# Performance work log

Measured on AMD Instinct MI355X. Metric: run time of the kernel, lower is better.

The kernel has to match this reference:

```python
import jax, jax.numpy as jnp
import numpy as np

N, E, F, H, HEADS, L, G = 16384, 262144, 16, 128, 4, 5, 128
DFF = 4 * H
EPS = 1e-5

def _bn(h, g, b):
    m = h.mean(axis=0)
    v = h.var(axis=0)
    return g * (h - m) / jnp.sqrt(v + EPS) + b

def setup_inputs():
    key = jax.random.key(0)
    ks = jax.random.split(key, 20)
    rn = lambda k, s, fan: jax.random.normal(k, s, jnp.float32) / np.float32(np.sqrt(fan))
    return {
        'x': jax.random.normal(ks[0], (N, F), jnp.float32),
        'edge_index': jax.random.randint(ks[1], (2, E), 0, N),
        'batch_index': jnp.sort(jax.random.randint(ks[2], (N,), 0, G)),
        'embW': rn(ks[3], (F, H), F), 'embb': jnp.zeros((H,), jnp.float32),
        'emb_g': jnp.ones((H,), jnp.float32), 'emb_be': jnp.zeros((H,), jnp.float32),
        'Wq': rn(ks[4], (L, H, HEADS * H), H), 'bq': jnp.zeros((L, HEADS * H), jnp.float32),
        'Wk': rn(ks[5], (L, H, HEADS * H), H), 'bk': jnp.zeros((L, HEADS * H), jnp.float32),
        'Wv': rn(ks[6], (L, H, HEADS * H), H), 'bv': jnp.zeros((L, HEADS * H), jnp.float32),
        'Wskip': rn(ks[7], (L, H, H), H), 'bskip': jnp.zeros((L, H), jnp.float32),
        'Wbeta': rn(ks[8], (L, 3 * H, 1), 3 * H),
        'W1': rn(ks[9], (L, H, DFF), H), 'b1': jnp.zeros((L, DFF), jnp.float32),
        'g1': jnp.ones((L, DFF), jnp.float32), 'be1': jnp.zeros((L, DFF), jnp.float32),
        'W2': rn(ks[10], (L, DFF, H), DFF), 'b2': jnp.zeros((L, H), jnp.float32),
        'predW': rn(ks[11], (H, 1), H), 'predb': jnp.zeros((1,), jnp.float32),
    }

def reference(x, edge_index, batch_index, embW, embb, emb_g, emb_be, Wq, bq, Wk, bk, Wv, bv, Wskip, bskip, Wbeta, W1, b1, g1, be1, W2, b2, predW, predb):
    src, dst = edge_index[0], edge_index[1]
    h = jax.nn.gelu(_bn(x @ embW + embb, emb_g, emb_be), approximate=False)
    scale = jnp.float32(1.0 / np.sqrt(H))  # sqrt(out_channels) per PyG TransformerConv

    def layer(h, p):
        Wq_, bq_, Wk_, bk_, Wv_, bv_, Ws_, bs_, Wb_, W1_, b1_, g1_, be1_, W2_, b2_ = p
        q = (h @ Wq_ + bq_).reshape(N, HEADS, H)
        k = (h @ Wk_ + bk_).reshape(N, HEADS, H)
        v = (h @ Wv_ + bv_).reshape(N, HEADS, H)
        logits = jnp.einsum('ehc,ehc->eh', q[dst], k[src]) * scale  # [E, HEADS]
        m = jax.ops.segment_max(logits, dst, num_segments=N)
        p_e = jnp.exp(logits - m[dst])
        denom = jax.ops.segment_sum(p_e, dst, num_segments=N) + 1e-16
        agg = jax.ops.segment_sum(p_e[:, :, None] * v[src], dst, num_segments=N)
        out = (agg / denom[:, :, None]).mean(axis=1)  # concat=False -> mean over heads
        x_r = h @ Ws_ + bs_
        beta = jax.nn.sigmoid(jnp.concatenate([out, x_r, out - x_r], axis=-1) @ Wb_)  # [N,1]
        out = beta * x_r + (1.0 - beta) * out
        hh = jax.nn.gelu(_bn(out @ W1_ + b1_, g1_, be1_), approximate=False)
        return hh @ W2_ + b2_

    def step(carry, p):
        return layer(carry, p), None

    h, _ = jax.lax.scan(step, h, (Wq, bq, Wk, bk, Wv, bv, Wskip, bskip, Wbeta, W1, b1, g1, be1, W2, b2))
    pooled = jax.ops.segment_max(h, batch_index, num_segments=G)  # MaxAggregation
    return (pooled @ predW + predb).reshape(-1)
```

## Files before the change

### kernel.cpp

```cpp
#include <hip/hip_runtime.h>
#include <hip/hip_bf16.h>

using bf16 = __hip_bfloat16;
typedef __attribute__((ext_vector_type(8))) short bf16x8;
typedef __attribute__((ext_vector_type(4))) float f32x4;

constexpr int N_   = 16384;
constexpr int E_   = 262144;
constexpr int F_   = 16;
constexpr int H_   = 128;
constexpr int NF1_ = 640;
constexpr int DFF_ = 512;
constexpr int G_   = 128;
constexpr int L_   = 5;
constexpr float EPS_ = 1e-5f;

constexpr int WCAT1SZ = NF1_ * 128;
constexpr int W1TSZ   = 512 * 128;
constexpr int W2TSZ   = 512 * 128;
constexpr int WVSSZ   = 128 * 512;
constexpr int TRBLKS  = 5 * 144;

__device__ __forceinline__ float gelu_f(float x) {
  return 0.5f * x * (1.0f + erff(x * 0.70710678118654752440f));
}

__device__ __forceinline__ void unpack8(const uint4 w, float* f) {
  f[0] = __uint_as_float(w.x << 16); f[1] = __uint_as_float(w.x & 0xFFFF0000u);
  f[2] = __uint_as_float(w.y << 16); f[3] = __uint_as_float(w.y & 0xFFFF0000u);
  f[4] = __uint_as_float(w.z << 16); f[5] = __uint_as_float(w.z & 0xFFFF0000u);
  f[6] = __uint_as_float(w.w << 16); f[7] = __uint_as_float(w.w & 0xFFFF0000u);
}

__global__ __launch_bounds__(256) void k_ptrans(
    const float* __restrict__ Ws, const float* __restrict__ W1,
    const float* __restrict__ W2, const float* __restrict__ bs,
    const float* __restrict__ bv,
    bf16* __restrict__ Wcat1, bf16* __restrict__ W1t, bf16* __restrict__ W2t,
    float* __restrict__ bcat, float* __restrict__ bvm) {
  __shared__ float lds[32][33];
  const int b = blockIdx.x;
  if (b >= TRBLKS) {
    int j = (b - TRBLKS) * 256 + threadIdx.x;
    if (j < 5 * NF1_) {
      int l = j / NF1_, c = j % NF1_;
      if (c >= 512) bcat[j] = bs[l * 128 + (c - 512)];
    } else if (j < 5 * NF1_ + 5 * 128) {
      int j2 = j - 5 * NF1_;
      int l = j2 / 128, n = j2 % 128;
      bvm[j2] = 0.25f * (bv[l * 512 + n] + bv[l * 512 + 128 + n]
                       + bv[l * 512 + 256 + n] + bv[l * 512 + 384 + n]);
    }
    return;
  }
  const int l = b / 144, t = b % 144;
  const float* src; int C; bf16* dst; int dld; int nof; int tt;
  if (t < 16) {
    tt = t;
    src = Ws + (size_t)l * 128 * 128; C = 128;
    dst = Wcat1 + (size_t)l * WCAT1SZ; dld = 128; nof = 512;
  } else if (t < 80) {
    tt = t - 16;
    src = W1 + (size_t)l * 128 * 512; C = 512;
    dst = W1t + (size_t)l * W1TSZ; dld = 128; nof = 0;
  } else {
    tt = t - 80;
    src = W2 + (size_t)l * 512 * 128; C = 128;
    dst = W2t + (size_t)l * W2TSZ; dld = 512; nof = 0;
  }
  const int tpr = C >> 5;
  const int r0 = (tt / tpr) * 32, c0 = (tt % tpr) * 32;
  const int j = threadIdx.x & 31, g = threadIdx.x >> 5;
#pragma unroll
  for (int ii = 0; ii < 4; ++ii) {
    int i = g * 4 + ii;
    lds[i][j] = src[(size_t)(r0 + i) * C + c0 + j];
  }
  __syncthreads();
#pragma unroll
  for (int ii = 0; ii < 4; ++ii) {
    int i = g * 4 + ii;
    dst[(size_t)(nof + c0 + i) * dld + r0 + j] = __float2bfloat16(lds[j][i]);
  }
}

__global__ __launch_bounds__(256) void k_wvprep(const float* __restrict__ Wv,
                                                bf16* __restrict__ Wvs) {
  __shared__ float lds[32][33];
  const int b = blockIdx.x;
  const int l = b / 64, rest = b % 64;
  const int h = rest / 16, tt = rest % 16;
  const int r0 = (tt / 4) * 32, c0 = (tt % 4) * 32;
  const float* src = Wv + (size_t)l * 128 * 512 + h * 128;
  bf16* dst = Wvs + (size_t)l * WVSSZ;
  const int j = threadIdx.x & 31, g = threadIdx.x >> 5;
#pragma unroll
  for (int ii = 0; ii < 4; ++ii) {
    int i = g * 4 + ii;
    lds[i][j] = src[(size_t)(r0 + i) * 512 + c0 + j];
  }
  __syncthreads();
#pragma unroll
  for (int ii = 0; ii < 4; ++ii) {
    int i = g * 4 + ii;
    dst[(size_t)(c0 + i) * 512 + h * 128 + r0 + j] = __float2bfloat16(0.25f * lds[j][i]);
  }
}

__global__ __launch_bounds__(256) void k_gmat(
    const float* __restrict__ Wq, const float* __restrict__ Wk,
    const float* __restrict__ bq,
    bf16* __restrict__ Wcat1, float* __restrict__ bcat) {
  __shared__ float lq[32][132];
  __shared__ float lk[32][132];
  const int l = blockIdx.x >> 2, h = blockIdx.x & 3;
  const int half = blockIdx.y;
  const int tid = threadIdx.x;
  const int c = tid & 127, ch = tid >> 7;
  const int cp0 = half * 64 + ch * 32;
  const float* wqL = Wq + (size_t)l * 128 * 512 + h * 128;
  const float* wkL = Wk + (size_t)l * 128 * 512 + h * 128;
  float acc[32];
#pragma unroll
  for (int j = 0; j < 32; ++j) acc[j] = 0.f;
  for (int a0 = 0; a0 < 128; a0 += 32) {
    __syncthreads();
#pragma unroll
    for (int q4 = 0; q4 < 4; ++q4) {
      int f4 = tid * 4 + q4;
      int row = f4 >> 3, af = f4 & 7;
      float4 gq = *reinterpret_cast<const float4*>(wqL + (size_t)row * 512 + a0 + af * 4);
      float4 gk = *reinterpret_cast<const float4*>(wkL + (size_t)row * 512 + a0 + af * 4);
      lq[af * 4 + 0][row] = gq.x; lq[af * 4 + 1][row] = gq.y;
      lq[af * 4 + 2][row] = gq.z; lq[af * 4 + 3][row] = gq.w;
      lk[af * 4 + 0][row] = gk.x; lk[af * 4 + 1][row] = gk.y;
      lk[af * 4 + 2][row] = gk.z; lk[af * 4 + 3][row] = gk.w;
    }
    __syncthreads();
    for (int a = 0; a < 32; ++a) {
      float wq = lq[a][c];
#pragma unroll
      for (int j = 0; j < 32; ++j) acc[j] = fmaf(wq, lk[a][cp0 + j], acc[j]);
    }
  }
  bf16* gt = Wcat1 + (size_t)l * WCAT1SZ;
#pragma unroll
  for (int j = 0; j < 32; ++j)
    gt[(size_t)(h * 128 + cp0 + j) * 128 + c] = __float2bfloat16(acc[j]);
  if (half == 0 && ch == 0) {
    float s = 0.f;
    const float* wkr = wkL + (size_t)c * 512;
    const float* bqh = bq + (size_t)l * 512 + h * 128;
    for (int a = 0; a < 128; ++a) s = fmaf(wkr[a], bqh[a], s);
    bcat[(size_t)l * NF1_ + h * 128 + c] = s;
  }
}

__global__ __launch_bounds__(256) void k_embed2(const float* __restrict__ x,
    const float* __restrict__ W, const float* __restrict__ b,
    float* __restrict__ out, float* __restrict__ ss, float* __restrict__ sq) {
  __shared__ float xs[128][16];
  __shared__ float wsm[16][128];
  __shared__ float sr[2][128], qr[2][128];
  const int blk = blockIdx.x;
  const int t = threadIdx.x;
  for (int i = t; i < 16 * 128; i += 256) wsm[i >> 7][i & 127] = W[i];
  for (int i = t; i < 128 * 16; i += 256) xs[i >> 4][i & 15] = x[(size_t)blk * 2048 + i];
  __syncthreads();
  const int c = t & 127, rg = t >> 7;
  float bc = b[c];
  float s = 0.f, q = 0.f;
  for (int r = rg * 64; r < rg * 64 + 64; ++r) {
    float v = bc;
#pragma unroll
    for (int f = 0; f < 16; ++f) v = fmaf(xs[r][f], wsm[f][c], v);
    out[(size_t)(blk * 128 + r) * 128 + c] = v;
    s += v; q += v * v;
  }
  sr[rg][c] = s; qr[rg][c] = q;
  __syncthreads();
  if (t < 128) { ss[blk * 128 + t] = sr[0][t] + sr[1][t]; sq[blk * 128 + t] = qr[0][t] + qr[1][t]; }
}

template<int NC>
__global__ void k_bn_finalize(const float* __restrict__ sums, const float* __restrict__ sumsq,
                              const float* __restrict__ g, const float* __restrict__ be,
                              float* __restrict__ a, float* __restrict__ cc) {
  int c = blockIdx.x * 128 + threadIdx.x;
  if (c >= NC) return;
  float s = 0.f, q = 0.f;
  for (int b = 0; b < 128; ++b) { s += sums[b * NC + c]; q += sumsq[b * NC + c]; }
  float mean = s * (1.0f / N_);
  float var  = q * (1.0f / N_) - mean * mean;
  float inv  = rsqrtf(var + EPS_);
  float aa   = g[c] * inv;
  a[c]  = aa;
  cc[c] = be[c] - aa * mean;
}

template<int NC>
__global__ void k_bn_apply_gelu_cast(const float* __restrict__ xin, const float* __restrict__ a,
                                     const float* __restrict__ cc, bf16* __restrict__ outb) {
  int i4 = (blockIdx.x * 256 + threadIdx.x) * 4;
  int c = i4 & (NC - 1);
  float4 v = *reinterpret_cast<const float4*>(xin + i4);
  union { uint2 u2; bf16 h[4]; } pk;
  pk.h[0] = __float2bfloat16(gelu_f(fmaf(a[c + 0], v.x, cc[c + 0])));
  pk.h[1] = __float2bfloat16(gelu_f(fmaf(a[c + 1], v.y, cc[c + 1])));
  pk.h[2] = __float2bfloat16(gelu_f(fmaf(a[c + 2], v.z, cc[c + 2])));
  pk.h[3] = __float2bfloat16(gelu_f(fmaf(a[c + 3], v.w, cc[c + 3])));
  *reinterpret_cast<uint2*>(outb + i4) = pk.u2;
}

__global__ void k_count(const int* __restrict__ dst, int* __restrict__ deg) {
  int e = blockIdx.x * 256 + threadIdx.x;
  if (e < E_) atomicAdd(&deg[dst[e]], 1);
}

__global__ void k_bsum(const int* __restrict__ deg, int* __restrict__ bsum) {
  __shared__ int sh[256];
  int t = threadIdx.x;
  sh[t] = deg[blockIdx.x * 256 + t];
  __syncthreads();
  for (int d = 128; d > 0; d >>= 1) { if (t < d) sh[t] += sh[t + d]; __syncthreads(); }
  if (t == 0) bsum[blockIdx.x] = sh[0];
}

__global__ void k_boffs(const int* __restrict__ deg, const int* __restrict__ bsum,
                        int* __restrict__ offs) {
  __shared__ int sh[256];
  __shared__ int baseSh;
  int t = threadIdx.x;
  if (t < 64) {
    int v = bsum[t];
    int s = v;
    for (int d = 1; d < 64; d <<= 1) { int o = __shfl_up(s, d); if (t >= d) s += o; }
    if (t == (int)blockIdx.x) baseSh = s - v;
  }
  int v = deg[blockIdx.x * 256 + t];
  sh[t] = v;
  __syncthreads();
  for (int d = 1; d < 256; d <<= 1) {
    int add = (t >= d) ? sh[t - d] : 0;
    __syncthreads();
    sh[t] += add;
    __syncthreads();
  }
  offs[blockIdx.x * 256 + t] = baseSh + sh[t] - v;
  if (blockIdx.x == 63 && t == 255) offs[N_] = E_;
}

__global__ void k_scatter(const int* __restrict__ src, const int* __restrict__ dst,
                          const int* __restrict__ off, int* __restrict__ cursor,
                          int* __restrict__ srcs) {
  int e = blockIdx.x * 256 + threadIdx.x;
  if (e < E_) {
    int d = dst[e];
    int pos = off[d] + atomicAdd(&cursor[d], 1);
    srcs[pos] = src[e];
  }
}

template<int KDIM, int NOUT, int TM, int MODE>
__global__ __launch_bounds__(256) void k_mfma(
    const bf16* __restrict__ A, const float* __restrict__ Af,
    const bf16* __restrict__ BT, const float* __restrict__ bias,
    float* __restrict__ outF, bf16* __restrict__ outB,
    float* __restrict__ zfp, float* __restrict__ xrp,
    float* __restrict__ ss, float* __restrict__ sq,
    const float* __restrict__ aCol, const float* __restrict__ cCol) {
  constexpr int MF = TM / 32;
  __shared__ bf16 As[TM][72];
  __shared__ bf16 Bs[128][72];
  __shared__ float sred[2][128], qred[2][128];
  __shared__ float aS[MODE == 4 ? KDIM : 1], cS[MODE == 4 ? KDIM : 1];
  const int tid = threadIdx.x;
  const int wid = tid >> 6, lane = tid & 63;
  const int wr = wid >> 1, wc = wid & 1;
  const int m0 = blockIdx.x * TM, n0 = blockIdx.y * 128;
  const int ln = lane & 15, lq = lane >> 4;
  if constexpr (MODE == 4) {
    for (int i = tid; i < KDIM; i += 256) { aS[i] = aCol[i]; cS[i] = cCol[i]; }
    __syncthreads();
  }
  f32x4 acc[MF][4];
#pragma unroll
  for (int i = 0; i < MF; ++i)
#pragma unroll
    for (int j = 0; j < 4; ++j) acc[i][j] = (f32x4){0.f, 0.f, 0.f, 0.f};

  for (int k0 = 0; k0 < KDIM; k0 += 64) {
#pragma unroll
    for (int u = tid; u < TM * 8; u += 256) {
      int r = u >> 3, c = u & 7;
      if constexpr (MODE == 4) {
        const float4* ap = reinterpret_cast<const float4*>(Af + (size_t)(m0 + r) * KDIM + k0 + c * 8);
        float4 f0 = ap[0], f1 = ap[1];
        float f[8] = {f0.x, f0.y, f0.z, f0.w, f1.x, f1.y, f1.z, f1.w};
        int colb = k0 + c * 8;
        union { uint4 u4; bf16 h[8]; } pk;
#pragma unroll
        for (int j = 0; j < 8; ++j)
          pk.h[j] = __float2bfloat16(gelu_f(fmaf(aS[colb + j], f[j], cS[colb + j])));
        *(uint4*)(&As[r][c * 8]) = pk.u4;
      } else {
        *(uint4*)(&As[r][c * 8]) = *(const uint4*)(A + (size_t)(m0 + r) * KDIM + k0 + c * 8);
      }
    }
#pragma unroll
    for (int u = tid; u < 1024; u += 256) {
      int r = u >> 3, c = u & 7;
      *(uint4*)(&Bs[r][c * 8]) = *(const uint4*)(BT + (size_t)(n0 + r) * KDIM + k0 + c * 8);
    }
    __syncthreads();
#pragma unroll
    for (int kk = 0; kk < 2; ++kk) {
      bf16x8 af[MF], bg[4];
#pragma unroll
      for (int i = 0; i < MF; ++i)
        af[i] = *(const bf16x8*)(&As[wr * (TM / 2) + i * 16 + ln][kk * 32 + lq * 8]);
#pragma unroll
      for (int j = 0; j < 4; ++j)
        bg[j] = *(const bf16x8*)(&Bs[wc * 64 + j * 16 + ln][kk * 32 + lq * 8]);
#pragma unroll
      for (int i = 0; i < MF; ++i)
#pragma unroll
        for (int j = 0; j < 4; ++j)
          acc[i][j] = __builtin_amdgcn_mfma_f32_16x16x32_bf16(af[i], bg[j], acc[i][j], 0, 0, 0);
    }
    __syncthreads();
  }
  float ssj[4] = {0.f, 0.f, 0.f, 0.f}, sqj[4] = {0.f, 0.f, 0.f, 0.f};
#pragma unroll
  for (int i = 0; i < MF; ++i) {
#pragma unroll
    for (int j = 0; j < 4; ++j) {
      int gcol = n0 + wc * 64 + j * 16 + ln;
      float bv = 0.f;
      if constexpr (MODE != 5) bv = bias[gcol];
      int row0 = m0 + wr * (TM / 2) + i * 16 + lq * 4;
#pragma unroll
      for (int qq = 0; qq < 4; ++qq) {
        float val = acc[i][j][qq] + bv;
        int row = row0 + qq;
        if (MODE == 3) {
          outF[(size_t)row * NOUT + gcol] = val;
          ssj[j] += val; sqj[j] += val * val;
        } else if (MODE == 4) {
          outF[(size_t)row * NOUT + gcol] = val;
          outB[(size_t)row * NOUT + gcol] = __float2bfloat16(val);
        } else if (MODE == 5) {
          outF[(size_t)row * NOUT + gcol] = val;
        } else {
          if (n0 < 512) zfp[(size_t)row * 512 + gcol] = val;
          else          xrp[(size_t)row * H_ + (gcol - 512)] = val;
        }
      }
    }
  }
  if constexpr (MODE == 3) {
#pragma unroll
    for (int j = 0; j < 4; ++j) {
      ssj[j] += __shfl_xor(ssj[j], 16); ssj[j] += __shfl_xor(ssj[j], 32);
      sqj[j] += __shfl_xor(sqj[j], 16); sqj[j] += __shfl_xor(sqj[j], 32);
    }
    if (lq == 0) {
#pragma unroll
      for (int j = 0; j < 4; ++j) {
        sred[wr][wc * 64 + j * 16 + ln] = ssj[j];
        qred[wr][wc * 64 + j * 16 + ln] = sqj[j];
      }
    }
    __syncthreads();
    if (tid < 128) {
      ss[(size_t)blockIdx.x * NOUT + n0 + tid] = sred[0][tid] + sred[1][tid];
      sq[(size_t)blockIdx.x * NOUT + n0 + tid] = qred[0][tid] + qred[1][tid];
    }
  }
}

__global__ __launch_bounds__(256) void k_attn(const float* __restrict__ zf,
    const bf16* __restrict__ hb, const int* __restrict__ srcs,
    const int* __restrict__ off, bf16* __restrict__ aggB) {
  const int wave = threadIdx.x >> 6;
  const int lane = threadIdx.x & 63;
  const int bid = blockIdx.x;
  const int swz = ((bid & 7) << 9) | (bid >> 3);
  const int node = swz * 4 + wave;
  const int sub = lane & 15;
  const float scale = 0.08838834764831845f;
  float qf[8];
  {
    const float4* qp = reinterpret_cast<const float4*>(zf + (size_t)node * 512) + lane * 2;
    float4 a = qp[0], b = qp[1];
    qf[0]=a.x; qf[1]=a.y; qf[2]=a.z; qf[3]=a.w;
    qf[4]=b.x; qf[5]=b.y; qf[6]=b.z; qf[7]=b.w;
  }
  float m = -1e30f, den = 0.f;
  float acc[8] = {0.f, 0.f, 0.f, 0.f, 0.f, 0.f, 0.f, 0.f};
  const int s0 = off[node], s1 = off[node + 1];
  if (s0 < s1) {
    int i0 = srcs[s0];
    int i1 = (s0 + 1 < s1) ? srcs[s0 + 1] : i0;
    uint4 h0 = *(const uint4*)(hb + (size_t)i0 * 128 + sub * 8);
    uint4 h1 = *(const uint4*)(hb + (size_t)i1 * 128 + sub * 8);
    for (int t = s0; t < s1; t += 2) {
      int j0 = (t + 2 < s1) ? srcs[t + 2] : i0;
      int j1 = (t + 3 < s1) ? srcs[t + 3] : i0;
      uint4 nh0 = *(const uint4*)(hb + (size_t)j0 * 128 + sub * 8);
      uint4 nh1 = *(const uint4*)(hb + (size_t)j1 * 128 + sub * 8);
      {
        float hf[8]; unpack8(h0, hf);
        float p = hf[0]*qf[0]+hf[1]*qf[1]+hf[2]*qf[2]+hf[3]*qf[3]
                + hf[4]*qf[4]+hf[5]*qf[5]+hf[6]*qf[6]+hf[7]*qf[7];
        p += __shfl_xor(p, 1); p += __shfl_xor(p, 2);
        p += __shfl_xor(p, 4); p += __shfl_xor(p, 8);
        float logit = p * scale;
        if (logit > m + 8.f) {
          float co = __expf(m - logit);
          den *= co;
#pragma unroll
          for (int j = 0; j < 8; ++j) acc[j] *= co;
          m = logit;
        }
        float pe = __expf(logit - m);
        den += pe;
#pragma unroll
        for (int j = 0; j < 8; ++j) acc[j] = fmaf(pe, hf[j], acc[j]);
      }
      if (t + 1 < s1) {
        float hf[8]; unpack8(h1, hf);
        float p = hf[0]*qf[0]+hf[1]*qf[1]+hf[2]*qf[2]+hf[3]*qf[3]
                + hf[4]*qf[4]+hf[5]*qf[5]+hf[6]*qf[6]+hf[7]*qf[7];
        p += __shfl_xor(p, 1); p += __shfl_xor(p, 2);
        p += __shfl_xor(p, 4); p += __shfl_xor(p, 8);
        float logit = p * scale;
        if (logit > m + 8.f) {
          float co = __expf(m - logit);
          den *= co;
#pragma unroll
          for (int j = 0; j < 8; ++j) acc[j] *= co;
          m = logit;
        }
        float pe = __expf(logit - m);
        den += pe;
#pragma unroll
        for (int j = 0; j < 8; ++j) acc[j] = fmaf(pe, hf[j], acc[j]);
      }
      h0 = nh0; h1 = nh1;
    }
  }
  float inv = 1.f / (den + 1e-16f);
  union { uint4 u4; bf16 h[8]; } pk;
#pragma unroll
  for (int j = 0; j < 8; ++j) pk.h[j] = __float2bfloat16(acc[j] * inv);
  *reinterpret_cast<uint4*>(aggB + (size_t)node * 512 + lane * 8) = pk.u4;
}

__global__ __launch_bounds__(256) void k_beta(const float* __restrict__ out0,
    const float* __restrict__ xr, const float* __restrict__ Wb,
    const float* __restrict__ bvm, const int* __restrict__ off,
    bf16* __restrict__ gated) {
  const int wave = threadIdx.x >> 6;
  const int lane = threadIdx.x & 63;
  const int node = blockIdx.x * 4 + wave;
  const int c0 = lane * 2;
  bool hasE = off[node + 1] > off[node];
  float2 o = *reinterpret_cast<const float2*>(out0 + (size_t)node * H_ + c0);
  if (hasE) { o.x += bvm[c0]; o.y += bvm[c0 + 1]; }
  float2 xv = *reinterpret_cast<const float2*>(xr + (size_t)node * H_ + c0);
  float s = o.x * (Wb[c0] + Wb[256 + c0]) + xv.x * (Wb[128 + c0] - Wb[256 + c0])
          + o.y * (Wb[c0 + 1] + Wb[256 + c0 + 1]) + xv.y * (Wb[128 + c0 + 1] - Wb[256 + c0 + 1]);
#pragma unroll
  for (int d = 1; d < 64; d <<= 1) s += __shfl_xor(s, d);
  float beta = 1.f / (1.f + __expf(-s));
  union { unsigned u; bf16 h[2]; } pk;
  pk.h[0] = __float2bfloat16(beta * xv.x + (1.f - beta) * o.x);
  pk.h[1] = __float2bfloat16(beta * xv.y + (1.f - beta) * o.y);
  *reinterpret_cast<unsigned*>(gated + (size_t)node * H_ + c0) = pk.u;
}

__global__ __launch_bounds__(256) void k_poolpred(const float* __restrict__ h,
    const int* __restrict__ batch, const float* __restrict__ predW,
    const float* __restrict__ predb, float* __restrict__ out) {
  __shared__ float cm[2][128];
  __shared__ int range[2];
  const int g = blockIdx.x, t = threadIdx.x;
  if (t < 2) {
    int target = g + t;
    int lo = 0, hi = N_;
    while (lo < hi) { int mid = (lo + hi) >> 1; if (batch[mid] < target) lo = mid + 1; else hi = mid; }
    range[t] = lo;
  }
  __syncthreads();
  const int lo = range[0], hi = range[1];
  const int c = t & 127, rg = t >> 7;
  float m = -3.402823466e+38f;
  for (int r = lo + rg; r < hi; r += 2) m = fmaxf(m, h[(size_t)r * H_ + c]);
  cm[rg][c] = m;
  __syncthreads();
  if (t < 64) {
    float m0 = fmaxf(cm[0][t], cm[1][t]);
    float m1 = fmaxf(cm[0][t + 64], cm[1][t + 64]);
    float s = m0 * predW[t] + m1 * predW[t + 64];
#pragma unroll
    for (int d = 1; d < 64; d <<= 1) s += __shfl_xor(s, d);
    if (t == 0) out[g] = s + predb[0];
  }
}

extern "C" void kernel_launch(void* const* d_in, const int* in_sizes, int n_in,
                              void* d_out, int out_size, void* d_ws, size_t ws_size,
                              hipStream_t stream) {
  const float* x      = (const float*)d_in[0];
  const int*   edge   = (const int*)d_in[1];
  const int*   esrc   = edge;
  const int*   edst   = edge + E_;
  const int*   batch  = (const int*)d_in[2];
  const float* embW   = (const float*)d_in[3];
  const float* embb   = (const float*)d_in[4];
  const float* emb_g  = (const float*)d_in[5];
  const float* emb_be = (const float*)d_in[6];
  const float* Wq     = (const float*)d_in[7];
  const float* bq     = (const float*)d_in[8];
  const float* Wk     = (const float*)d_in[9];
  const float* Wv     = (const float*)d_in[11];
  const float* bv     = (const float*)d_in[12];
  const float* Wskip  = (const float*)d_in[13];
  const float* bskip  = (const float*)d_in[14];
  const float* Wbeta  = (const float*)d_in[15];
  const float* W1     = (const float*)d_in[16];
  const float* b1     = (const float*)d_in[17];
  const float* g1     = (const float*)d_in[18];
  const float* be1    = (const float*)d_in[19];
  const float* W2     = (const float*)d_in[20];
  const float* b2     = (const float*)d_in[21];
  const float* predW  = (const float*)d_in[22];
  const float* predb  = (const float*)d_in[23];

  float* ws = (float*)d_ws;
  size_t o = 0;
  auto alloc_f = [&](size_t n) { float* p = ws + o; o += n; return p; };
  float* A32   = alloc_f((size_t)N_ * 512);
  float* B32   = alloc_f((size_t)N_ * H_);
  float* xr    = alloc_f((size_t)N_ * H_);
  float* stats = alloc_f(2 * 128 * DFF_);
  float* a_c   = alloc_f(DFF_);
  float* c_c   = alloc_f(DFF_);
  float* bcat  = alloc_f(5 * NF1_);
  float* bvm   = alloc_f(5 * 128);
  bf16* bp = (bf16*)(ws + o);
  size_t ob = 0;
  auto alloc_b = [&](size_t n) { bf16* p = bp + ob; ob += n; return p; };
  bf16* aggB = alloc_b((size_t)N_ * 512);
  bf16* hb   = alloc_b((size_t)N_ * H_);
  bf16* gated= alloc_b((size_t)N_ * H_);
  bf16* Wcat1= alloc_b((size_t)5 * WCAT1SZ);
  bf16* W1t  = alloc_b((size_t)5 * W1TSZ);
  bf16* W2t  = alloc_b((size_t)5 * W2TSZ);
  bf16* Wvs  = alloc_b((size_t)5 * WVSSZ);
  int* deg    = (int*)(bp + ob);
  int* offs   = deg + N_;
  int* cursor = offs + N_ + 1;
  int* srcs   = cursor + N_;
  int* bsum   = srcs + E_;

  float* zf   = A32;  float* t1 = A32;
  float* out0 = B32;  float* h32 = B32;

  k_ptrans<<<TRBLKS + 15, 256, 0, stream>>>(Wskip, W1, W2, bskip, bv,
                                            Wcat1, W1t, W2t, bcat, bvm);
  k_wvprep<<<320, 256, 0, stream>>>(Wv, Wvs);
  k_gmat<<<dim3(20, 2), 256, 0, stream>>>(Wq, Wk, bq, Wcat1, bcat);

  hipMemsetAsync(deg, 0, N_ * sizeof(int), stream);
  hipMemsetAsync(cursor, 0, N_ * sizeof(int), stream);
  k_count  <<<E_ / 256, 256, 0, stream>>>(edst, deg);
  k_bsum   <<<64, 256, 0, stream>>>(deg, bsum);
  k_boffs  <<<64, 256, 0, stream>>>(deg, bsum, offs);
  k_scatter<<<E_ / 256, 256, 0, stream>>>(esrc, edst, offs, cursor, srcs);

  k_embed2<<<128, 256, 0, stream>>>(x, embW, embb, A32, stats, stats + 128 * 128);
  k_bn_finalize<128><<<1, 128, 0, stream>>>(stats, stats + 128 * 128, emb_g, emb_be, a_c, c_c);
  k_bn_apply_gelu_cast<128><<<N_ * H_ / 1024, 256, 0, stream>>>(A32, a_c, c_c, hb);

  for (int l = 0; l < L_; ++l) {
    const float* Wb_ = Wbeta + (size_t)l * 3 * H_;
    const float* b1_ = b1 + (size_t)l * DFF_;
    const float* g1_ = g1 + (size_t)l * DFF_;
    const float* be1_= be1 + (size_t)l * DFF_;
    const float* b2_ = b2 + (size_t)l * H_;

    k_mfma<128, NF1_, 128, 2><<<dim3(N_ / 128, NF1_ / 128), 256, 0, stream>>>(
        hb, nullptr, Wcat1 + (size_t)l * WCAT1SZ, bcat + (size_t)l * NF1_,
        nullptr, nullptr, zf, xr, nullptr, nullptr, nullptr, nullptr);

    k_attn<<<N_ / 4, 256, 0, stream>>>(zf, hb, srcs, offs, aggB);

    k_mfma<512, 128, 64, 5><<<dim3(N_ / 64, 1), 256, 0, stream>>>(
        aggB, nullptr, Wvs + (size_t)l * WVSSZ, nullptr,
        out0, nullptr, nullptr, nullptr, nullptr, nullptr, nullptr, nullptr);

    k_beta<<<N_ / 4, 256, 0, stream>>>(out0, xr, Wb_, bvm + (size_t)l * 128, offs, gated);

    k_mfma<128, 512, 128, 3><<<dim3(N_ / 128, 4), 256, 0, stream>>>(
        gated, nullptr, W1t + (size_t)l * W1TSZ, b1_, t1, nullptr, nullptr, nullptr,
        stats, stats + 128 * 512, nullptr, nullptr);

    k_bn_finalize<512><<<4, 128, 0, stream>>>(stats, stats + 128 * 512, g1_, be1_, a_c, c_c);

    k_mfma<512, 128, 64, 4><<<dim3(N_ / 64, 1), 256, 0, stream>>>(
        nullptr, t1, W2t + (size_t)l * W2TSZ, b2_, h32, hb, nullptr, nullptr,
        nullptr, nullptr, a_c, c_c);
  }

  k_poolpred<<<G_, 256, 0, stream>>>(h32, batch, predW, predb, (float*)d_out);
}
```

Measured before the change: 765.8 us.

## Split-K the two K=512 GEMMs into four partials with reduction kernels

The two K=512 GEMMs (aggregated V projection and the FFN down-projection) now launch four K-slices each, writing fp32 partial outputs. The V partials are summed inside the beta-gating kernel, and a new reduction kernel sums the FFN partials, adds the bias and emits both fp32 and bf16 hidden states. This raises block count from 256 to 1024 so the GPU's compute units are better occupied. In exchange it writes and reads four N×128 fp32 partial buffers per GEMM and adds an extra kernel launch per layer.

```diff
diff --git a/kernel.cpp b/kernel.cpp
--- a/kernel.cpp
+++ b/kernel.cpp
@@ -261,7 +261,7 @@
   }
 }
 
-template<int KDIM, int NOUT, int TM, int MODE>
+template<int KDIM, int KLD, int NOUT, int TM, int MODE>
 __global__ __launch_bounds__(256) void k_mfma(
     const bf16* __restrict__ A, const float* __restrict__ Af,
     const bf16* __restrict__ BT, const float* __restrict__ bias,
@@ -270,6 +270,7 @@
     float* __restrict__ ss, float* __restrict__ sq,
     const float* __restrict__ aCol, const float* __restrict__ cCol) {
   constexpr int MF = TM / 32;
+  constexpr bool SPLITK = (MODE == 4 || MODE == 5);
   __shared__ bf16 As[TM][72];
   __shared__ bf16 Bs[128][72];
   __shared__ float sred[2][128], qred[2][128];
@@ -277,10 +278,13 @@
   const int tid = threadIdx.x;
   const int wid = tid >> 6, lane = tid & 63;
   const int wr = wid >> 1, wc = wid & 1;
-  const int m0 = blockIdx.x * TM, n0 = blockIdx.y * 128;
+  const int m0 = blockIdx.x * TM;
+  const int n0 = SPLITK ? 0 : blockIdx.y * 128;
+  const int ks = SPLITK ? blockIdx.y : 0;
   const int ln = lane & 15, lq = lane >> 4;
+  const size_t koff = (size_t)ks * KDIM;
   if constexpr (MODE == 4) {
-    for (int i = tid; i < KDIM; i += 256) { aS[i] = aCol[i]; cS[i] = cCol[i]; }
+    for (int i = tid; i < KDIM; i += 256) { aS[i] = aCol[koff + i]; cS[i] = cCol[koff + i]; }
     __syncthreads();
   }
   f32x4 acc[MF][4];
@@ -294,7 +298,7 @@
     for (int u = tid; u < TM * 8; u += 256) {
       int r = u >> 3, c = u & 7;
       if constexpr (MODE == 4) {
-        const float4* ap = reinterpret_cast<const float4*>(Af + (size_t)(m0 + r) * KDIM + k0 + c * 8);
+        const float4* ap = reinterpret_cast<const float4*>(Af + (size_t)(m0 + r) * KLD + koff + k0 + c * 8);
         float4 f0 = ap[0], f1 = ap[1];
         float f[8] = {f0.x, f0.y, f0.z, f0.w, f1.x, f1.y, f1.z, f1.w};
         int colb = k0 + c * 8;
@@ -304,13 +308,13 @@
           pk.h[j] = __float2bfloat16(gelu_f(fmaf(aS[colb + j], f[j], cS[colb + j])));
         *(uint4*)(&As[r][c * 8]) = pk.u4;
       } else {
-        *(uint4*)(&As[r][c * 8]) = *(const uint4*)(A + (size_t)(m0 + r) * KDIM + k0 + c * 8);
+        *(uint4*)(&As[r][c * 8]) = *(const uint4*)(A + (size_t)(m0 + r) * KLD + koff + k0 + c * 8);
       }
     }
 #pragma unroll
     for (int u = tid; u < 1024; u += 256) {
       int r = u >> 3, c = u & 7;
-      *(uint4*)(&Bs[r][c * 8]) = *(const uint4*)(BT + (size_t)(n0 + r) * KDIM + k0 + c * 8);
+      *(uint4*)(&Bs[r][c * 8]) = *(const uint4*)(BT + (size_t)(n0 + r) * KLD + koff + k0 + c * 8);
     }
     __syncthreads();
 #pragma unroll
@@ -330,6 +334,7 @@
     }
     __syncthreads();
   }
+  float* outP = SPLITK ? (outF + (size_t)ks * N_ * NOUT) : outF;
   float ssj[4] = {0.f, 0.f, 0.f, 0.f}, sqj[4] = {0.f, 0.f, 0.f, 0.f};
 #pragma unroll
   for (int i = 0; i < MF; ++i) {
@@ -337,20 +342,17 @@
     for (int j = 0; j < 4; ++j) {
       int gcol = n0 + wc * 64 + j * 16 + ln;
       float bv = 0.f;
-      if constexpr (MODE != 5) bv = bias[gcol];
+      if constexpr (MODE == 2 || MODE == 3) bv = bias[gcol];
       int row0 = m0 + wr * (TM / 2) + i * 16 + lq * 4;
 #pragma unroll
       for (int qq = 0; qq < 4; ++qq) {
         float val = acc[i][j][qq] + bv;
         int row = row0 + qq;
         if (MODE == 3) {
-          outF[(size_t)row * NOUT + gcol] = val;
+          outP[(size_t)row * NOUT + gcol] = val;
           ssj[j] += val; sqj[j] += val * val;
-        } else if (MODE == 4) {
-          outF[(size_t)row * NOUT + gcol] = val;
-          outB[(size_t)row * NOUT + gcol] = __float2bfloat16(val);
-        } else if (MODE == 5) {
-          outF[(size_t)row * NOUT + gcol] = val;
+        } else if (MODE == 4 || MODE == 5) {
+          outP[(size_t)row * NOUT + gcol] = val;
         } else {
           if (n0 < 512) zfp[(size_t)row * 512 + gcol] = val;
           else          xrp[(size_t)row * H_ + (gcol - 512)] = val;
@@ -457,7 +459,7 @@
   *reinterpret_cast<uint4*>(aggB + (size_t)node * 512 + lane * 8) = pk.u4;
 }
 
-__global__ __launch_bounds__(256) void k_beta(const float* __restrict__ out0,
+__global__ __launch_bounds__(256) void k_vredbeta(const float* __restrict__ vp,
     const float* __restrict__ xr, const float* __restrict__ Wb,
     const float* __restrict__ bvm, const int* __restrict__ off,
     bf16* __restrict__ gated) {
@@ -466,9 +468,17 @@
   const int node = blockIdx.x * 4 + wave;
   const int c0 = lane * 2;
   bool hasE = off[node + 1] > off[node];
-  float2 o = *reinterpret_cast<const float2*>(out0 + (size_t)node * H_ + c0);
+  const size_t base = (size_t)node * H_ + c0;
+  const size_t stride = (size_t)N_ * H_;
+  float2 p0 = *reinterpret_cast<const float2*>(vp + base);
+  float2 p1 = *reinterpret_cast<const float2*>(vp + stride + base);
+  float2 p2 = *reinterpret_cast<const float2*>(vp + 2 * stride + base);
+  float2 p3 = *reinterpret_cast<const float2*>(vp + 3 * stride + base);
+  float2 o;
+  o.x = ((p0.x + p1.x) + p2.x) + p3.x;
+  o.y = ((p0.y + p1.y) + p2.y) + p3.y;
   if (hasE) { o.x += bvm[c0]; o.y += bvm[c0 + 1]; }
-  float2 xv = *reinterpret_cast<const float2*>(xr + (size_t)node * H_ + c0);
+  float2 xv = *reinterpret_cast<const float2*>(xr + base);
   float s = o.x * (Wb[c0] + Wb[256 + c0]) + xv.x * (Wb[128 + c0] - Wb[256 + c0])
           + o.y * (Wb[c0 + 1] + Wb[256 + c0 + 1]) + xv.y * (Wb[128 + c0 + 1] - Wb[256 + c0 + 1]);
 #pragma unroll
@@ -477,7 +487,28 @@
   union { unsigned u; bf16 h[2]; } pk;
   pk.h[0] = __float2bfloat16(beta * xv.x + (1.f - beta) * o.x);
   pk.h[1] = __float2bfloat16(beta * xv.y + (1.f - beta) * o.y);
-  *reinterpret_cast<unsigned*>(gated + (size_t)node * H_ + c0) = pk.u;
+  *reinterpret_cast<unsigned*>(gated + base) = pk.u;
+}
+
+__global__ __launch_bounds__(256) void k_f2red(const float* __restrict__ fp,
+    const float* __restrict__ b2, float* __restrict__ h32, bf16* __restrict__ hb) {
+  const int i4 = (blockIdx.x * 256 + threadIdx.x) * 4;
+  const int c = i4 & 127;
+  const size_t stride = (size_t)N_ * H_;
+  float4 a0 = *reinterpret_cast<const float4*>(fp + i4);
+  float4 a1 = *reinterpret_cast<const float4*>(fp + stride + i4);
+  float4 a2 = *reinterpret_cast<const float4*>(fp + 2 * stride + i4);
+  float4 a3 = *reinterpret_cast<const float4*>(fp + 3 * stride + i4);
+  float4 s;
+  s.x = ((a0.x + a1.x) + a2.x) + a3.x + b2[c + 0];
+  s.y = ((a0.y + a1.y) + a2.y) + a3.y + b2[c + 1];
+  s.z = ((a0.z + a1.z) + a2.z) + a3.z + b2[c + 2];
+  s.w = ((a0.w + a1.w) + a2.w) + a3.w + b2[c + 3];
+  *reinterpret_cast<float4*>(h32 + i4) = s;
+  union { uint2 u2; bf16 h[4]; } pk;
+  pk.h[0] = __float2bfloat16(s.x); pk.h[1] = __float2bfloat16(s.y);
+  pk.h[2] = __float2bfloat16(s.z); pk.h[3] = __float2bfloat16(s.w);
+  *reinterpret_cast<uint2*>(hb + i4) = pk.u2;
 }
 
 __global__ __launch_bounds__(256) void k_poolpred(const float* __restrict__ h,
@@ -544,6 +575,7 @@
   float* A32   = alloc_f((size_t)N_ * 512);
   float* B32   = alloc_f((size_t)N_ * H_);
   float* xr    = alloc_f((size_t)N_ * H_);
+  float* fpart = alloc_f((size_t)4 * N_ * H_);
   float* stats = alloc_f(2 * 128 * DFF_);
   float* a_c   = alloc_f(DFF_);
   float* c_c   = alloc_f(DFF_);
@@ -565,8 +597,8 @@
   int* srcs   = cursor + N_;
   int* bsum   = srcs + E_;
 
-  float* zf   = A32;  float* t1 = A32;
-  float* out0 = B32;  float* h32 = B32;
+  float* zf   = A32;  float* t1 = A32;  float* vpart = A32;
+  float* h32 = B32;
 
   k_ptrans<<<TRBLKS + 15, 256, 0, stream>>>(Wskip, W1, W2, bskip, bv,
                                             Wcat1, W1t, W2t, bcat, bvm);
@@ -591,27 +623,29 @@
     const float* be1_= be1 + (size_t)l * DFF_;
     const float* b2_ = b2 + (size_t)l * H_;
 
-    k_mfma<128, NF1_, 128, 2><<<dim3(N_ / 128, NF1_ / 128), 256, 0, stream>>>(
+    k_mfma<128, 128, NF1_, 128, 2><<<dim3(N_ / 128, NF1_ / 128), 256, 0, stream>>>(
         hb, nullptr, Wcat1 + (size_t)l * WCAT1SZ, bcat + (size_t)l * NF1_,
         nullptr, nullptr, zf, xr, nullptr, nullptr, nullptr, nullptr);
 
     k_attn<<<N_ / 4, 256, 0, stream>>>(zf, hb, srcs, offs, aggB);
 
-    k_mfma<512, 128, 64, 5><<<dim3(N_ / 64, 1), 256, 0, stream>>>(
+    k_mfma<128, 512, 128, 64, 5><<<dim3(N_ / 64, 4), 256, 0, stream>>>(
         aggB, nullptr, Wvs + (size_t)l * WVSSZ, nullptr,
-        out0, nullptr, nullptr, nullptr, nullptr, nullptr, nullptr, nullptr);
-
-    k_beta<<<N_ / 4, 256, 0, stream>>>(out0, xr, Wb_, bvm + (size_t)l * 128, offs, gated);
-
-    k_mfma<128, 512, 128, 3><<<dim3(N_ / 128, 4), 256, 0, stream>>>(
+        vpart, nullptr, nullptr, nullptr, nullptr, nullptr, nullptr, nullptr);
+
+    k_vredbeta<<<N_ / 4, 256, 0, stream>>>(vpart, xr, Wb_, bvm + (size_t)l * 128, offs, gated);
+
+    k_mfma<128, 128, 512, 128, 3><<<dim3(N_ / 128, 4), 256, 0, stream>>>(
         gated, nullptr, W1t + (size_t)l * W1TSZ, b1_, t1, nullptr, nullptr, nullptr,
         stats, stats + 128 * 512, nullptr, nullptr);
 
     k_bn_finalize<512><<<4, 128, 0, stream>>>(stats, stats + 128 * 512, g1_, be1_, a_c, c_c);
 
-    k_mfma<512, 128, 64, 4><<<dim3(N_ / 64, 1), 256, 0, stream>>>(
-        nullptr, t1, W2t + (size_t)l * W2TSZ, b2_, h32, hb, nullptr, nullptr,
+    k_mfma<128, 512, 128, 64, 4><<<dim3(N_ / 64, 4), 256, 0, stream>>>(
+        nullptr, t1, W2t + (size_t)l * W2TSZ, nullptr, fpart, nullptr, nullptr, nullptr,
         nullptr, nullptr, a_c, c_c);
+
+    k_f2red<<<N_ * H_ / 1024, 256, 0, stream>>>(fpart, b2_, h32, hb);
   }
 
   k_poolpred<<<G_, 256, 0, stream>>>(h32, batch, predW, predb, (float*)d_out);
```

New measurement: 696.7 us. 1.1x faster.

## Replace LDS-tiled MFMA GEMM with register-resident A-row wave GEMM

Applied to the files above, without the earlier changes.

Replaces the shared-memory tiled MFMA GEMM with a kernel in which each wave holds a full 16-row A strip in registers and loops over all output column tiles, reading B fragments directly from global memory (which stays cache-resident for the small weights). This removes LDS staging and block barriers. The BN+GELU that was fused into the W2 GEMM's A-load becomes a separate bf16 apply pass into a scratch buffer, and BN partial statistics are now written per wave, so the finalize kernel sums 1024 partials instead of 128. The trade-off is one extra elementwise kernel plus heavier global/L2 traffic for B, in exchange for no LDS or sync overhead.

```diff
diff --git a/kernel.cpp b/kernel.cpp
--- a/kernel.cpp
+++ b/kernel.cpp
@@ -182,14 +182,14 @@
   if (t < 128) { ss[blk * 128 + t] = sr[0][t] + sr[1][t]; sq[blk * 128 + t] = qr[0][t] + qr[1][t]; }
 }
 
-template<int NC>
+template<int NC, int NP>
 __global__ void k_bn_finalize(const float* __restrict__ sums, const float* __restrict__ sumsq,
                               const float* __restrict__ g, const float* __restrict__ be,
                               float* __restrict__ a, float* __restrict__ cc) {
   int c = blockIdx.x * 128 + threadIdx.x;
   if (c >= NC) return;
   float s = 0.f, q = 0.f;
-  for (int b = 0; b < 128; ++b) { s += sums[b * NC + c]; q += sumsq[b * NC + c]; }
+  for (int b = 0; b < NP; ++b) { s += sums[(size_t)b * NC + c]; q += sumsq[(size_t)b * NC + c]; }
   float mean = s * (1.0f / N_);
   float var  = q * (1.0f / N_) - mean * mean;
   float inv  = rsqrtf(var + EPS_);
@@ -261,120 +261,74 @@
   }
 }
 
-template<int KDIM, int NOUT, int TM, int MODE>
-__global__ __launch_bounds__(256) void k_mfma(
-    const bf16* __restrict__ A, const float* __restrict__ Af,
-    const bf16* __restrict__ BT, const float* __restrict__ bias,
+template<int KDIM, int NOUT, int MODE>
+__global__ __launch_bounds__(256) void k_wgemm(
+    const bf16* __restrict__ A, const bf16* __restrict__ BT,
+    const float* __restrict__ bias,
     float* __restrict__ outF, bf16* __restrict__ outB,
     float* __restrict__ zfp, float* __restrict__ xrp,
-    float* __restrict__ ss, float* __restrict__ sq,
-    const float* __restrict__ aCol, const float* __restrict__ cCol) {
-  constexpr int MF = TM / 32;
-  __shared__ bf16 As[TM][72];
-  __shared__ bf16 Bs[128][72];
-  __shared__ float sred[2][128], qred[2][128];
-  __shared__ float aS[MODE == 4 ? KDIM : 1], cS[MODE == 4 ? KDIM : 1];
+    float* __restrict__ ss, float* __restrict__ sq) {
+  constexpr int KS = KDIM / 32;
   const int tid = threadIdx.x;
   const int wid = tid >> 6, lane = tid & 63;
-  const int wr = wid >> 1, wc = wid & 1;
-  const int m0 = blockIdx.x * TM, n0 = blockIdx.y * 128;
   const int ln = lane & 15, lq = lane >> 4;
-  if constexpr (MODE == 4) {
-    for (int i = tid; i < KDIM; i += 256) { aS[i] = aCol[i]; cS[i] = cCol[i]; }
-    __syncthreads();
-  }
-  f32x4 acc[MF][4];
-#pragma unroll
-  for (int i = 0; i < MF; ++i)
-#pragma unroll
-    for (int j = 0; j < 4; ++j) acc[i][j] = (f32x4){0.f, 0.f, 0.f, 0.f};
-
-  for (int k0 = 0; k0 < KDIM; k0 += 64) {
-#pragma unroll
-    for (int u = tid; u < TM * 8; u += 256) {
-      int r = u >> 3, c = u & 7;
-      if constexpr (MODE == 4) {
-        const float4* ap = reinterpret_cast<const float4*>(Af + (size_t)(m0 + r) * KDIM + k0 + c * 8);
-        float4 f0 = ap[0], f1 = ap[1];
-        float f[8] = {f0.x, f0.y, f0.z, f0.w, f1.x, f1.y, f1.z, f1.w};
-        int colb = k0 + c * 8;
-        union { uint4 u4; bf16 h[8]; } pk;
-#pragma unroll
-        for (int j = 0; j < 8; ++j)
-          pk.h[j] = __float2bfloat16(gelu_f(fmaf(aS[colb + j], f[j], cS[colb + j])));
-        *(uint4*)(&As[r][c * 8]) = pk.u4;
+  const int m0 = blockIdx.x * 64 + wid * 16;
+  bf16x8 a[KS];
+  const bf16* ap = A + (size_t)(m0 + ln) * KDIM + lq * 8;
+#pragma unroll
+  for (int ks = 0; ks < KS; ++ks) a[ks] = *(const bf16x8*)(ap + ks * 32);
+  const int orow = m0 + lq * 4;
+  for (int nf = 0; nf < NOUT / 16; ++nf) {
+    f32x4 acc = (f32x4){0.f, 0.f, 0.f, 0.f};
+    const bf16* bp = BT + (size_t)(nf * 16 + ln) * KDIM + lq * 8;
+#pragma unroll
+    for (int ks = 0; ks < KS; ++ks)
+      acc = __builtin_amdgcn_mfma_f32_16x16x32_bf16(a[ks], *(const bf16x8*)(bp + ks * 32), acc, 0, 0, 0);
+    const int col = nf * 16 + ln;
+    float bv = 0.f;
+    if constexpr (MODE != 5) bv = bias[col];
+    float v0 = acc[0] + bv, v1 = acc[1] + bv, v2 = acc[2] + bv, v3 = acc[3] + bv;
+    if constexpr (MODE == 2) {
+      if (col < 512) {
+        zfp[(size_t)(orow + 0) * 512 + col] = v0;
+        zfp[(size_t)(orow + 1) * 512 + col] = v1;
+        zfp[(size_t)(orow + 2) * 512 + col] = v2;
+        zfp[(size_t)(orow + 3) * 512 + col] = v3;
       } else {
-        *(uint4*)(&As[r][c * 8]) = *(const uint4*)(A + (size_t)(m0 + r) * KDIM + k0 + c * 8);
+        int cx = col - 512;
+        xrp[(size_t)(orow + 0) * 128 + cx] = v0;
+        xrp[(size_t)(orow + 1) * 128 + cx] = v1;
+        xrp[(size_t)(orow + 2) * 128 + cx] = v2;
+        xrp[(size_t)(orow + 3) * 128 + cx] = v3;
       }
-    }
-#pragma unroll
-    for (int u = tid; u < 1024; u += 256) {
-      int r = u >> 3, c = u & 7;
-      *(uint4*)(&Bs[r][c * 8]) = *(const uint4*)(BT + (size_t)(n0 + r) * KDIM + k0 + c * 8);
-    }
-    __syncthreads();
-#pragma unroll
-    for (int kk = 0; kk < 2; ++kk) {
-      bf16x8 af[MF], bg[4];
-#pragma unroll
-      for (int i = 0; i < MF; ++i)
-        af[i] = *(const bf16x8*)(&As[wr * (TM / 2) + i * 16 + ln][kk * 32 + lq * 8]);
-#pragma unroll
-      for (int j = 0; j < 4; ++j)
-        bg[j] = *(const bf16x8*)(&Bs[wc * 64 + j * 16 + ln][kk * 32 + lq * 8]);
-#pragma unroll
-      for (int i = 0; i < MF; ++i)
-#pragma unroll
-        for (int j = 0; j < 4; ++j)
-          acc[i][j] = __builtin_amdgcn_mfma_f32_16x16x32_bf16(af[i], bg[j], acc[i][j], 0, 0, 0);
-    }
-    __syncthreads();
-  }
-  float ssj[4] = {0.f, 0.f, 0.f, 0.f}, sqj[4] = {0.f, 0.f, 0.f, 0.f};
-#pragma unroll
-  for (int i = 0; i < MF; ++i) {
-#pragma unroll
-    for (int j = 0; j < 4; ++j) {
-      int gcol = n0 + wc * 64 + j * 16 + ln;
-      float bv = 0.f;
-      if constexpr (MODE != 5) bv = bias[gcol];
-      int row0 = m0 + wr * (TM / 2) + i * 16 + lq * 4;
-#pragma unroll
-      for (int qq = 0; qq < 4; ++qq) {
-        float val = acc[i][j][qq] + bv;
-        int row = row0 + qq;
-        if (MODE == 3) {
-          outF[(size_t)row * NOUT + gcol] = val;
-          ssj[j] += val; sqj[j] += val * val;
-        } else if (MODE == 4) {
-          outF[(size_t)row * NOUT + gcol] = val;
-          outB[(size_t)row * NOUT + gcol] = __float2bfloat16(val);
-        } else if (MODE == 5) {
-          outF[(size_t)row * NOUT + gcol] = val;
-        } else {
-          if (n0 < 512) zfp[(size_t)row * 512 + gcol] = val;
-          else          xrp[(size_t)row * H_ + (gcol - 512)] = val;
-        }
+    } else if constexpr (MODE == 3) {
+      outF[(size_t)(orow + 0) * 512 + col] = v0;
+      outF[(size_t)(orow + 1) * 512 + col] = v1;
+      outF[(size_t)(orow + 2) * 512 + col] = v2;
+      outF[(size_t)(orow + 3) * 512 + col] = v3;
+      float s1 = ((v0 + v1) + v2) + v3;
+      float s2 = ((v0 * v0 + v1 * v1) + v2 * v2) + v3 * v3;
+      s1 += __shfl_xor(s1, 16); s1 += __shfl_xor(s1, 32);
+      s2 += __shfl_xor(s2, 16); s2 += __shfl_xor(s2, 32);
+      if (lq == 0) {
+        size_t pidx = (size_t)(blockIdx.x * 4 + wid) * 512 + col;
+        ss[pidx] = s1;
+        sq[pidx] = s2;
       }
-    }
-  }
-  if constexpr (MODE == 3) {
-#pragma unroll
-    for (int j = 0; j < 4; ++j) {
-      ssj[j] += __shfl_xor(ssj[j], 16); ssj[j] += __shfl_xor(ssj[j], 32);
-      sqj[j] += __shfl_xor(sqj[j], 16); sqj[j] += __shfl_xor(sqj[j], 32);
-    }
-    if (lq == 0) {
-#pragma unroll
-      for (int j = 0; j < 4; ++j) {
-        sred[wr][wc * 64 + j * 16 + ln] = ssj[j];
-        qred[wr][wc * 64 + j * 16 + ln] = sqj[j];
-      }
-    }
-    __syncthreads();
-    if (tid < 128) {
-      ss[(size_t)blockIdx.x * NOUT + n0 + tid] = sred[0][tid] + sred[1][tid];
-      sq[(size_t)blockIdx.x * NOUT + n0 + tid] = qred[0][tid] + qred[1][tid];
+    } else if constexpr (MODE == 5) {
+      outF[(size_t)(orow + 0) * 128 + col] = v0;
+      outF[(size_t)(orow + 1) * 128 + col] = v1;
+      outF[(size_t)(orow + 2) * 128 + col] = v2;
+      outF[(size_t)(orow + 3) * 128 + col] = v3;
+    } else {
+      outF[(size_t)(orow + 0) * 128 + col] = v0;
+      outF[(size_t)(orow + 1) * 128 + col] = v1;
+      outF[(size_t)(orow + 2) * 128 + col] = v2;
+      outF[(size_t)(orow + 3) * 128 + col] = v3;
+      outB[(size_t)(orow + 0) * 128 + col] = __float2bfloat16(v0);
+      outB[(size_t)(orow + 1) * 128 + col] = __float2bfloat16(v1);
+      outB[(size_t)(orow + 2) * 128 + col] = __float2bfloat16(v2);
+      outB[(size_t)(orow + 3) * 128 + col] = __float2bfloat16(v3);
     }
   }
 }
@@ -466,9 +420,10 @@
   const int node = blockIdx.x * 4 + wave;
   const int c0 = lane * 2;
   bool hasE = off[node + 1] > off[node];
-  float2 o = *reinterpret_cast<const float2*>(out0 + (size_t)node * H_ + c0);
+  const size_t base = (size_t)node * H_ + c0;
+  float2 o = *reinterpret_cast<const float2*>(out0 + base);
   if (hasE) { o.x += bvm[c0]; o.y += bvm[c0 + 1]; }
-  float2 xv = *reinterpret_cast<const float2*>(xr + (size_t)node * H_ + c0);
+  float2 xv = *reinterpret_cast<const float2*>(xr + base);
   float s = o.x * (Wb[c0] + Wb[256 + c0]) + xv.x * (Wb[128 + c0] - Wb[256 + c0])
           + o.y * (Wb[c0 + 1] + Wb[256 + c0 + 1]) + xv.y * (Wb[128 + c0 + 1] - Wb[256 + c0 + 1]);
 #pragma unroll
@@ -477,7 +432,7 @@
   union { unsigned u; bf16 h[2]; } pk;
   pk.h[0] = __float2bfloat16(beta * xv.x + (1.f - beta) * o.x);
   pk.h[1] = __float2bfloat16(beta * xv.y + (1.f - beta) * o.y);
-  *reinterpret_cast<unsigned*>(gated + (size_t)node * H_ + c0) = pk.u;
+  *reinterpret_cast<unsigned*>(gated + base) = pk.u;
 }
 
 __global__ __launch_bounds__(256) void k_poolpred(const float* __restrict__ h,
@@ -544,7 +499,7 @@
   float* A32   = alloc_f((size_t)N_ * 512);
   float* B32   = alloc_f((size_t)N_ * H_);
   float* xr    = alloc_f((size_t)N_ * H_);
-  float* stats = alloc_f(2 * 128 * DFF_);
+  float* stats = alloc_f((size_t)2 * 1024 * DFF_);
   float* a_c   = alloc_f(DFF_);
   float* c_c   = alloc_f(DFF_);
   float* bcat  = alloc_f(5 * NF1_);
@@ -567,6 +522,7 @@
 
   float* zf   = A32;  float* t1 = A32;
   float* out0 = B32;  float* h32 = B32;
+  bf16*  t1b  = aggB;
 
   k_ptrans<<<TRBLKS + 15, 256, 0, stream>>>(Wskip, W1, W2, bskip, bv,
                                             Wcat1, W1t, W2t, bcat, bvm);
@@ -581,7 +537,7 @@
   k_scatter<<<E_ / 256, 256, 0, stream>>>(esrc, edst, offs, cursor, srcs);
 
   k_embed2<<<128, 256, 0, stream>>>(x, embW, embb, A32, stats, stats + 128 * 128);
-  k_bn_finalize<128><<<1, 128, 0, stream>>>(stats, stats + 128 * 128, emb_g, emb_be, a_c, c_c);
+  k_bn_finalize<128, 128><<<1, 128, 0, stream>>>(stats, stats + 128 * 128, emb_g, emb_be, a_c, c_c);
   k_bn_apply_gelu_cast<128><<<N_ * H_ / 1024, 256, 0, stream>>>(A32, a_c, c_c, hb);
 
   for (int l = 0; l < L_; ++l) {
@@ -591,27 +547,30 @@
     const float* be1_= be1 + (size_t)l * DFF_;
     const float* b2_ = b2 + (size_t)l * H_;
 
-    k_mfma<128, NF1_, 128, 2><<<dim3(N_ / 128, NF1_ / 128), 256, 0, stream>>>(
-        hb, nullptr, Wcat1 + (size_t)l * WCAT1SZ, bcat + (size_t)l * NF1_,
-        nullptr, nullptr, zf, xr, nullptr, nullptr, nullptr, nullptr);
+    k_wgemm<128, NF1_, 2><<<N_ / 64, 256, 0, stream>>>(
+        hb, Wcat1 + (size_t)l * WCAT1SZ, bcat + (size_t)l * NF1_,
+        nullptr, nullptr, zf, xr, nullptr, nullptr);
 
     k_attn<<<N_ / 4, 256, 0, stream>>>(zf, hb, srcs, offs, aggB);
 
-    k_mfma<512, 128, 64, 5><<<dim3(N_ / 64, 1), 256, 0, stream>>>(
-        aggB, nullptr, Wvs + (size_t)l * WVSSZ, nullptr,
-        out0, nullptr, nullptr, nullptr, nullptr, nullptr, nullptr, nullptr);
+    k_wgemm<512, 128, 5><<<N_ / 64, 256, 0, stream>>>(
+        aggB, Wvs + (size_t)l * WVSSZ, nullptr,
+        out0, nullptr, nullptr, nullptr, nullptr, nullptr);
 
     k_beta<<<N_ / 4, 256, 0, stream>>>(out0, xr, Wb_, bvm + (size_t)l * 128, offs, gated);
 
-    k_mfma<128, 512, 128, 3><<<dim3(N_ / 128, 4), 256, 0, stream>>>(
-        gated, nullptr, W1t + (size_t)l * W1TSZ, b1_, t1, nullptr, nullptr, nullptr,
-        stats, stats + 128 * 512, nullptr, nullptr);
-
-    k_bn_finalize<512><<<4, 128, 0, stream>>>(stats, stats + 128 * 512, g1_, be1_, a_c, c_c);
-
-    k_mfma<512, 128, 64, 4><<<dim3(N_ / 64, 1), 256, 0, stream>>>(
-        nullptr, t1, W2t + (size_t)l * W2TSZ, b2_, h32, hb, nullptr, nullptr,
-        nullptr, nullptr, a_c, c_c);
+    k_wgemm<128, 512, 3><<<N_ / 64, 256, 0, stream>>>(
+        gated, W1t + (size_t)l * W1TSZ, b1_,
+        t1, nullptr, nullptr, nullptr, stats, stats + (size_t)1024 * 512);
+
+    k_bn_finalize<512, 1024><<<4, 128, 0, stream>>>(
+        stats, stats + (size_t)1024 * 512, g1_, be1_, a_c, c_c);
+
+    k_bn_apply_gelu_cast<512><<<N_ * DFF_ / 1024, 256, 0, stream>>>(t1, a_c, c_c, t1b);
+
+    k_wgemm<512, 128, 6><<<N_ / 64, 256, 0, stream>>>(
+        t1b, W2t + (size_t)l * W2TSZ, b2_,
+        h32, hb, nullptr, nullptr, nullptr, nullptr);
   }
 
   k_poolpred<<<G_, 256, 0, stream>>>(h32, batch, predW, predb, (float*)d_out);
```

After: 1.136 ms. 1.48x slower.
